# Optimization experiments

Hardware: AMD Instinct MI355X
Metric: run time of the kernel (lower is better)

The kernel has to match this reference:

```python
import jax, jax.numpy as jnp
import numpy as np

B, T, S, E, H = 4, 2048, 2048, 512, 8
D = E // H  # head_dim = 64
BIFURCATION_FACTOR = 1.0


def setup_inputs() -> dict:
    key = jax.random.key(0)
    ks = jax.random.split(key, 12)
    s = 1.0 / np.sqrt(E)
    return {
        "query": jax.random.normal(ks[0], (B, T, E), jnp.float32),
        "key_": jax.random.normal(ks[1], (B, S, E), jnp.float32),
        "value": jax.random.normal(ks[2], (B, S, E), jnp.float32),
        "Wq": jax.random.uniform(ks[3], (E, E), jnp.float32, -s, s),
        "bq": jax.random.uniform(ks[4], (E,), jnp.float32, -s, s),
        "Wk": jax.random.uniform(ks[5], (E, E), jnp.float32, -s, s),
        "bk": jax.random.uniform(ks[6], (E,), jnp.float32, -s, s),
        "Wv": jax.random.uniform(ks[7], (E, E), jnp.float32, -s, s),
        "bv": jax.random.uniform(ks[8], (E,), jnp.float32, -s, s),
        "Wo": jax.random.uniform(ks[9], (E, E), jnp.float32, -s, s),
        "bo": jax.random.uniform(ks[10], (E,), jnp.float32, -s, s),
        "r": jnp.asarray(3.5, jnp.float32),
    }


def _logistic_map(x, r):
    # sigmoid-normalize then one logistic-map iteration with learned r
    xn = jax.nn.sigmoid(x)
    r_scaled = BIFURCATION_FACTOR * jax.nn.sigmoid(r) * 4.0
    return r_scaled * xn * (1.0 - xn)


def reference(query, key_, value, Wq, bq, Wk, bk, Wv, bv, Wo, bo, r):
    q = _logistic_map(query @ Wq.T + bq, r)   # [B,T,E]
    k = _logistic_map(key_ @ Wk.T + bk, r)    # [B,S,E]
    v = value @ Wv.T + bv                     # [B,S,E]

    q = q.reshape(B, T, H, D).transpose(0, 2, 1, 3)  # [B,H,T,D]
    k = k.reshape(B, S, H, D).transpose(0, 2, 1, 3)  # [B,H,S,D]
    v = v.reshape(B, S, H, D).transpose(0, 2, 1, 3)  # [B,H,S,D]

    scores = jnp.einsum('bhtd,bhsd->bhts', q, k) / jnp.sqrt(jnp.asarray(D, q.dtype))
    attn = jax.nn.softmax(scores, axis=-1)           # [B,H,T,S]
    out = jnp.einsum('bhts,bhsd->bhtd', attn, v)     # [B,H,T,D]
    out = out.transpose(0, 2, 1, 3).reshape(B, T, E)
    return out @ Wo.T + bo
```

## Files before the change

### kernel.cpp

```cpp
#include <hip/hip_runtime.h>
#include <stdint.h>

#define B_ 4
#define T_ 2048
#define S_ 2048
#define E_ 512
#define H_ 8
#define D_ 64

using bf16x8 = __attribute__((ext_vector_type(8))) short;
using bf16x4 = __attribute__((ext_vector_type(4))) short;
using f32x4  = __attribute__((ext_vector_type(4))) float;

__device__ __forceinline__ unsigned short f2bf(float f) {
  unsigned u = __float_as_uint(f);
  u += 0x7fffu + ((u >> 16) & 1u);
  return (unsigned short)(u >> 16);
}

__device__ __forceinline__ float sigmoidf_(float x) {
  return 1.0f / (1.0f + __expf(-x));
}

__device__ __forceinline__ f32x4 mfma16x16x16(bf16x4 a, bf16x4 b, f32x4 c) {
#if __has_builtin(__builtin_amdgcn_mfma_f32_16x16x16bf16_1k)
  return __builtin_amdgcn_mfma_f32_16x16x16bf16_1k(a, b, c, 0, 0, 0);
#else
  asm("v_mfma_f32_16x16x16_bf16 %0, %1, %2, %0" : "+v"(c) : "v"(a), "v"(b));
  return c;
#endif
}

__device__ __forceinline__ void gl16(const void* g, void* l) {
  __builtin_amdgcn_global_load_lds(
      (const __attribute__((address_space(1))) unsigned*)g,
      (__attribute__((address_space(3))) unsigned*)l,
      16, 0, 0);
}

__device__ __forceinline__ int swzi(int row, int ebyte) {
  return row * 64 + ((ebyte ^ ((row & 7) << 4)) >> 1);
}

__global__ __launch_bounds__(256) void cvt_all(
    const float* __restrict__ q, const float* __restrict__ k, const float* __restrict__ v,
    const float* __restrict__ wq, const float* __restrict__ wk,
    const float* __restrict__ wv, const float* __restrict__ wo,
    unsigned short* __restrict__ oq, unsigned short* __restrict__ ok,
    unsigned short* __restrict__ ov, unsigned short* __restrict__ owq,
    unsigned short* __restrict__ owk, unsigned short* __restrict__ owv,
    unsigned short* __restrict__ owo) {
  const float* in; unsigned short* out; int n4, b, nb;
  int blk = blockIdx.x;
  if (blk < 1536) {
    int s = blk >> 9;
    in = (s == 0) ? q : (s == 1) ? k : v;
    out = (s == 0) ? oq : (s == 1) ? ok : ov;
    n4 = (B_ * T_ * E_) / 4; b = blk & 511; nb = 512;
  } else {
    int s = (blk - 1536) >> 5;
    in = (s == 0) ? wq : (s == 1) ? wk : (s == 2) ? wv : wo;
    out = (s == 0) ? owq : (s == 1) ? owk : (s == 2) ? owv : owo;
    n4 = (E_ * E_) / 4; b = (blk - 1536) & 31; nb = 32;
  }
  for (int i = b * 256 + threadIdx.x; i < n4; i += nb * 256) {
    float4 vv = ((const float4*)in)[i];
    ushort4 o;
    o.x = f2bf(vv.x); o.y = f2bf(vv.y); o.z = f2bf(vv.z); o.w = f2bf(vv.w);
    ((ushort4*)out)[i] = o;
  }
}

__global__ __launch_bounds__(256) void gemm_out(
    const unsigned short* __restrict__ A,
    const unsigned short* __restrict__ W,
    const float* __restrict__ bias,
    float* __restrict__ outp) {
  __shared__ unsigned short As[2][128 * 64];
  __shared__ unsigned short Bs[2][64 * 64];

  int bid = ((blockIdx.x & 7) << 6) + (blockIdx.x >> 3);
  int tid = threadIdx.x;
  int lane = tid & 63, wid = tid >> 6;
  int bm = bid >> 3, bn = bid & 7;
  int m0 = bm * 128, n0 = bn * 64;

  f32x4 acc[4][2] = {};

  int rowc = tid >> 3;
  int kswz = ((tid & 7) ^ (rowc & 7)) << 4;

  auto stage = [&](int buf, int kt) {
#pragma unroll
    for (int c = 0; c < 4; ++c) {
      const char* ga = (const char*)A + (size_t)(m0 + c * 32 + rowc) * 1024 + kt * 128 + kswz;
      gl16(ga, (char*)&As[buf][0] + c * 4096 + (wid << 10));
    }
#pragma unroll
    for (int c = 0; c < 2; ++c) {
      const char* gw = (const char*)W + (size_t)(n0 + c * 32 + rowc) * 1024 + kt * 128 + kswz;
      gl16(gw, (char*)&Bs[buf][0] + c * 4096 + (wid << 10));
    }
  };

  stage(0, 0);

  int wm = wid >> 1, wn = wid & 1;
  int fr = lane & 15, fg = lane >> 4;

  for (int kt = 0; kt < 8; ++kt) {
    __syncthreads();
    if (kt < 7) stage((kt + 1) & 1, kt + 1);
    int buf = kt & 1;
#pragma unroll
    for (int ks = 0; ks < 2; ++ks) {
      bf16x8 a[4], b[2];
#pragma unroll
      for (int mi = 0; mi < 4; ++mi)
        a[mi] = *(const bf16x8*)&As[buf][swzi(wm * 64 + mi * 16 + fr, ks * 64 + fg * 16)];
#pragma unroll
      for (int ni = 0; ni < 2; ++ni)
        b[ni] = *(const bf16x8*)&Bs[buf][swzi(wn * 32 + ni * 16 + fr, ks * 64 + fg * 16)];
#pragma unroll
      for (int mi = 0; mi < 4; ++mi)
#pragma unroll
        for (int ni = 0; ni < 2; ++ni)
          acc[mi][ni] = __builtin_amdgcn_mfma_f32_16x16x32_bf16(a[mi], b[ni], acc[mi][ni], 0, 0, 0);
    }
  }

#pragma unroll
  for (int mi = 0; mi < 4; ++mi)
#pragma unroll
    for (int ni = 0; ni < 2; ++ni)
#pragma unroll
      for (int i = 0; i < 4; ++i) {
        int gm = m0 + wm * 64 + mi * 16 + fg * 4 + i;
        int gn = n0 + wn * 32 + ni * 16 + fr;
        outp[(size_t)gm * E_ + gn] = acc[mi][ni][i] + bias[gn];
      }
}

__global__ __launch_bounds__(256) void gemm_proj(
    const unsigned short* __restrict__ Aq, const unsigned short* __restrict__ Wqp,
    const float* __restrict__ bqp, unsigned short* __restrict__ oq,
    const unsigned short* __restrict__ Ak, const unsigned short* __restrict__ Wkp,
    const float* __restrict__ bkp, unsigned short* __restrict__ ok,
    const unsigned short* __restrict__ Av, const unsigned short* __restrict__ Wvp,
    const float* __restrict__ bvp, unsigned short* __restrict__ ov,
    const float* __restrict__ rptr, float sclq) {
  __shared__ unsigned short As[2][128 * 64];
  __shared__ unsigned short Bs[2][64 * 64];

  int job = blockIdx.x >> 9;
  int x = blockIdx.x & 511;
  int bid = ((x & 7) << 6) + (x >> 3);
  const unsigned short* A = (job == 0) ? Aq : (job == 1) ? Ak : Av;
  const unsigned short* W = (job == 0) ? Wqp : (job == 1) ? Wkp : Wvp;
  const float* bias = (job == 0) ? bqp : (job == 1) ? bkp : bvp;
  unsigned short* outp = (job == 0) ? oq : (job == 1) ? ok : ov;

  int bm, bn;
  if (job == 2) { bm = bid >> 7; bn = bid & 127; }
  else          { bm = bid >> 3; bn = bid & 7; }
  int m0 = bm * 128, n0 = bn * 64;

  f32x4 acc[4][2] = {};

  int tid = threadIdx.x;
  int lane = tid & 63, wid = tid >> 6;
  int rowc = tid >> 3;
  int kswz = ((tid & 7) ^ (rowc & 7)) << 4;

  auto stage = [&](int buf, int kt) {
#pragma unroll
    for (int c = 0; c < 4; ++c) {
      const char* ga = (const char*)A + (size_t)(m0 + c * 32 + rowc) * 1024 + kt * 128 + kswz;
      gl16(ga, (char*)&As[buf][0] + c * 4096 + (wid << 10));
    }
#pragma unroll
    for (int c = 0; c < 2; ++c) {
      const char* gw = (const char*)W + (size_t)(n0 + c * 32 + rowc) * 1024 + kt * 128 + kswz;
      gl16(gw, (char*)&Bs[buf][0] + c * 4096 + (wid << 10));
    }
  };

  stage(0, 0);

  int wm = wid >> 1, wn = wid & 1;
  int fr = lane & 15, fg = lane >> 4;

  for (int kt = 0; kt < 8; ++kt) {
    __syncthreads();
    if (kt < 7) stage((kt + 1) & 1, kt + 1);
    int buf = kt & 1;
#pragma unroll
    for (int ks = 0; ks < 2; ++ks) {
      bf16x8 a[4], b[2];
#pragma unroll
      for (int mi = 0; mi < 4; ++mi)
        a[mi] = *(const bf16x8*)&As[buf][swzi(wm * 64 + mi * 16 + fr, ks * 64 + fg * 16)];
#pragma unroll
      for (int ni = 0; ni < 2; ++ni)
        b[ni] = *(const bf16x8*)&Bs[buf][swzi(wn * 32 + ni * 16 + fr, ks * 64 + fg * 16)];
#pragma unroll
      for (int mi = 0; mi < 4; ++mi)
#pragma unroll
        for (int ni = 0; ni < 2; ++ni)
          acc[mi][ni] = __builtin_amdgcn_mfma_f32_16x16x32_bf16(a[mi], b[ni], acc[mi][ni], 0, 0, 0);
    }
  }

  float rs = 4.0f * sigmoidf_(rptr[0]) * ((job == 0) ? sclq : 1.0f);

#pragma unroll
  for (int mi = 0; mi < 4; ++mi) {
#pragma unroll
    for (int ni = 0; ni < 2; ++ni) {
#pragma unroll
      for (int i = 0; i < 4; ++i) {
        int gm = m0 + wm * 64 + mi * 16 + fg * 4 + i;
        int gn = n0 + wn * 32 + ni * 16 + fr;
        float v = acc[mi][ni][i];
        if (job < 2) {
          v += bias[gn];
          float xn = sigmoidf_(v);
          float val = rs * xn * (1.0f - xn);
          int b = gm >> 11, t = gm & 2047, h = gn >> 6, d = gn & 63;
          outp[((size_t)(b * H_ + h) * T_ + t) * D_ + d] = f2bf(val);
        } else {
          v += bias[gm];
          int h = gm >> 6, d = gm & 63, b = gn >> 11, s = gn & 2047;
          outp[((size_t)(b * H_ + h) * D_ + d) * S_ + s] = f2bf(v);
        }
      }
    }
  }
}

template <int CBa, int CBb>
__device__ __forceinline__ void tile_pair(
    char* sm, int koff0, int koff1, const int (&voff)[4],
    const bf16x8 (&qa)[2][2], f32x4 (&acco)[2][4], float (&lst)[2]) {
  union PU { unsigned u[2]; bf16x4 v; };

  bf16x8 ka[4][2];
#pragma unroll
  for (int ni = 0; ni < 4; ++ni) {
    ka[ni][0] = *(const bf16x8*)(sm + CBa + ni * 2048 + koff0);
    ka[ni][1] = *(const bf16x8*)(sm + CBa + ni * 2048 + koff1);
  }
  f32x4 sta[4][2] = {};
  __builtin_amdgcn_s_setprio(1);
#pragma unroll
  for (int ni = 0; ni < 4; ++ni)
#pragma unroll
    for (int mi = 0; mi < 2; ++mi) {
      sta[ni][mi] = __builtin_amdgcn_mfma_f32_16x16x32_bf16(ka[ni][0], qa[mi][0], sta[ni][mi], 0, 0, 0);
      sta[ni][mi] = __builtin_amdgcn_mfma_f32_16x16x32_bf16(ka[ni][1], qa[mi][1], sta[ni][mi], 0, 0, 0);
    }
  __builtin_amdgcn_s_setprio(0);

  bf16x8 kb[4][2];
#pragma unroll
  for (int ni = 0; ni < 4; ++ni) {
    kb[ni][0] = *(const bf16x8*)(sm + CBb + ni * 2048 + koff0);
    kb[ni][1] = *(const bf16x8*)(sm + CBb + ni * 2048 + koff1);
  }
  f32x4 stb[4][2] = {};
  __builtin_amdgcn_s_setprio(1);
#pragma unroll
  for (int ni = 0; ni < 4; ++ni)
#pragma unroll
    for (int mi = 0; mi < 2; ++mi) {
      stb[ni][mi] = __builtin_amdgcn_mfma_f32_16x16x32_bf16(kb[ni][0], qa[mi][0], stb[ni][mi], 0, 0, 0);
      stb[ni][mi] = __builtin_amdgcn_mfma_f32_16x16x32_bf16(kb[ni][1], qa[mi][1], stb[ni][mi], 0, 0, 0);
    }
  __builtin_amdgcn_s_setprio(0);

  bf16x4 pfa[2][4];
#pragma unroll
  for (int mi = 0; mi < 2; ++mi) {
    float sum = 0.f;
#pragma unroll
    for (int ni = 0; ni < 4; ++ni) {
      float p0 = __builtin_amdgcn_exp2f(sta[ni][mi][0]);
      float p1 = __builtin_amdgcn_exp2f(sta[ni][mi][1]);
      float p2 = __builtin_amdgcn_exp2f(sta[ni][mi][2]);
      float p3 = __builtin_amdgcn_exp2f(sta[ni][mi][3]);
      sum += (p0 + p1) + (p2 + p3);
      PU pu;
      asm("v_cvt_pk_bf16_f32 %0, %1, %2" : "=v"(pu.u[0]) : "v"(p0), "v"(p1));
      asm("v_cvt_pk_bf16_f32 %0, %1, %2" : "=v"(pu.u[1]) : "v"(p2), "v"(p3));
      pfa[mi][ni] = pu.v;
    }
    sum += __shfl_xor(sum, 16);
    sum += __shfl_xor(sum, 32);
    lst[mi] += sum;
  }

  __builtin_amdgcn_s_setprio(1);
#pragma unroll
  for (int nd = 0; nd < 4; ++nd)
#pragma unroll
    for (int ni = 0; ni < 4; ++ni) {
      bf16x4 vf = *(const bf16x4*)(sm + CBa + nd * 2048 + voff[ni]);
#pragma unroll
      for (int mi = 0; mi < 2; ++mi)
        acco[mi][nd] = mfma16x16x16(vf, pfa[mi][ni], acco[mi][nd]);
    }
  __builtin_amdgcn_s_setprio(0);

  bf16x4 pfb[2][4];
#pragma unroll
  for (int mi = 0; mi < 2; ++mi) {
    float sum = 0.f;
#pragma unroll
    for (int ni = 0; ni < 4; ++ni) {
      float p0 = __builtin_amdgcn_exp2f(stb[ni][mi][0]);
      float p1 = __builtin_amdgcn_exp2f(stb[ni][mi][1]);
      float p2 = __builtin_amdgcn_exp2f(stb[ni][mi][2]);
      float p3 = __builtin_amdgcn_exp2f(stb[ni][mi][3]);
      sum += (p0 + p1) + (p2 + p3);
      PU pu;
      asm("v_cvt_pk_bf16_f32 %0, %1, %2" : "=v"(pu.u[0]) : "v"(p0), "v"(p1));
      asm("v_cvt_pk_bf16_f32 %0, %1, %2" : "=v"(pu.u[1]) : "v"(p2), "v"(p3));
      pfb[mi][ni] = pu.v;
    }
    sum += __shfl_xor(sum, 16);
    sum += __shfl_xor(sum, 32);
    lst[mi] += sum;
  }

  __builtin_amdgcn_s_setprio(1);
#pragma unroll
  for (int nd = 0; nd < 4; ++nd)
#pragma unroll
    for (int ni = 0; ni < 4; ++ni) {
      bf16x4 vf = *(const bf16x4*)(sm + CBb + nd * 2048 + voff[ni]);
#pragma unroll
      for (int mi = 0; mi < 2; ++mi)
        acco[mi][nd] = mfma16x16x16(vf, pfb[mi][ni], acco[mi][nd]);
    }
  __builtin_amdgcn_s_setprio(0);
}

__global__ __launch_bounds__(256) void attn_flash(
    const unsigned short* __restrict__ qp,
    const unsigned short* __restrict__ kp,
    const unsigned short* __restrict__ vtp,
    unsigned short* __restrict__ attno) {
  __shared__ __align__(16) char smem[65536];

  int tid = threadIdx.x, lane = tid & 63, wid = tid >> 6;
  int wgid = ((blockIdx.x & 7) << 6) + (blockIdx.x >> 3);
  int tt = wgid & 15, bh = wgid >> 4;
  const char* qh = (const char*)qp + ((size_t)bh * T_ + tt * 128) * 128;
  const char* kh = (const char*)kp + (size_t)bh * S_ * 128;
  const char* vh = (const char*)vtp + (size_t)bh * D_ * S_ * 2;

  int rowc = tid >> 3;
  int kswz = ((tid & 7) ^ (rowc & 7)) << 4;

#define STAGE_K(SB, IT) { \
    gl16(kh + (size_t)((IT) * 64 + rowc) * 128 + kswz, smem + (SB) + (wid << 10)); \
    gl16(kh + (size_t)((IT) * 64 + 32 + rowc) * 128 + kswz, smem + (SB) + 4096 + (wid << 10)); }
#define STAGE_V(SB, IT) { \
    gl16(vh + (size_t)rowc * 4096 + (IT) * 128 + kswz, smem + (SB) + 8192 + (wid << 10)); \
    gl16(vh + (size_t)(32 + rowc) * 4096 + (IT) * 128 + kswz, smem + (SB) + 12288 + (wid << 10)); }

  STAGE_K(0, 0) STAGE_V(0, 0) STAGE_K(16384, 1) STAGE_V(16384, 1)
#pragma unroll
  for (int c = 0; c < 4; ++c)
    gl16(qh + (size_t)(c * 32 + rowc) * 128 + kswz, smem + 49152 + c * 4096 + (wid << 10));

  int fr = lane & 15, fg = (lane >> 4) & 3;
  int qrb = wid * 32;
  int koff0 = fr * 128 + ((fg * 16) ^ ((fr & 7) << 4));
  int koff1 = fr * 128 + ((64 + fg * 16) ^ ((fr & 7) << 4));
  int voff[4];
#pragma unroll
  for (int ni = 0; ni < 4; ++ni)
    voff[ni] = 8192 + fr * 128 + ((ni * 32 + fg * 8) ^ ((fr & 7) << 4));

  __syncthreads();

  bf16x8 qa[2][2];
#pragma unroll
  for (int mi = 0; mi < 2; ++mi) {
    qa[mi][0] = *(const bf16x8*)(smem + 49152 + (qrb + mi * 16) * 128 + koff0);
    qa[mi][1] = *(const bf16x8*)(smem + 49152 + (qrb + mi * 16) * 128 + koff1);
  }
  __syncthreads();

  f32x4 acco[2][4] = {};
  float lst[2] = {0.f, 0.f};

  STAGE_K(32768, 2) STAGE_V(32768, 2) STAGE_K(49152, 3) STAGE_V(49152, 3)
  tile_pair<0, 16384>(smem, koff0, koff1, voff, qa, acco, lst);

#pragma unroll 1
  for (int pp = 1; pp <= 7; ++pp) {
    int ta = pp * 4;
    __syncthreads();
    STAGE_K(0, ta) STAGE_V(0, ta) STAGE_K(16384, ta + 1) STAGE_V(16384, ta + 1)
    tile_pair<32768, 49152>(smem, koff0, koff1, voff, qa, acco, lst);
    __syncthreads();
    STAGE_K(32768, ta + 2) STAGE_V(32768, ta + 2) STAGE_K(49152, ta + 3) STAGE_V(49152, ta + 3)
    tile_pair<0, 16384>(smem, koff0, koff1, voff, qa, acco, lst);
  }
  __syncthreads();
  tile_pair<32768, 49152>(smem, koff0, koff1, voff, qa, acco, lst);

  int b = bh >> 3, h = bh & 7;
#pragma unroll
  for (int mi = 0; mi < 2; ++mi) {
    float rl = 1.0f / lst[mi];
    int t = tt * 128 + qrb + mi * 16 + fr;
    unsigned short* rowp = attno + (size_t)(b * T_ + t) * E_ + h * 64;
#pragma unroll
    for (int nd = 0; nd < 4; ++nd) {
      ushort4 o;
      o.x = f2bf(acco[mi][nd][0] * rl);
      o.y = f2bf(acco[mi][nd][1] * rl);
      o.z = f2bf(acco[mi][nd][2] * rl);
      o.w = f2bf(acco[mi][nd][3] * rl);
      *(ushort4*)(rowp + nd * 16 + fg * 4) = o;
    }
  }
#undef STAGE_K
#undef STAGE_V
}

extern "C" void kernel_launch(void* const* d_in, const int* in_sizes, int n_in,
                              void* d_out, int out_size, void* d_ws, size_t ws_size,
                              hipStream_t stream) {
  const float* query = (const float*)d_in[0];
  const float* key_  = (const float*)d_in[1];
  const float* value = (const float*)d_in[2];
  const float* Wq    = (const float*)d_in[3];
  const float* bq    = (const float*)d_in[4];
  const float* Wk    = (const float*)d_in[5];
  const float* bk    = (const float*)d_in[6];
  const float* Wv    = (const float*)d_in[7];
  const float* bv    = (const float*)d_in[8];
  const float* Wo    = (const float*)d_in[9];
  const float* bo    = (const float*)d_in[10];
  const float* r     = (const float*)d_in[11];

  char* ws = (char*)d_ws;
  unsigned short* qb    = (unsigned short*)(ws + 0);
  unsigned short* kb    = (unsigned short*)(ws + 8388608);
  unsigned short* vb    = (unsigned short*)(ws + 16777216);
  unsigned short* wqb   = (unsigned short*)(ws + 25165824);
  unsigned short* wkb   = (unsigned short*)(ws + 25690112);
  unsigned short* wvb   = (unsigned short*)(ws + 26214400);
  unsigned short* wob   = (unsigned short*)(ws + 26738688);
  unsigned short* qp    = (unsigned short*)(ws + 27262976);
  unsigned short* kp    = (unsigned short*)(ws + 35651584);
  unsigned short* vtp   = (unsigned short*)(ws + 44040192);
  unsigned short* attno = (unsigned short*)(ws + 52428800);

  cvt_all<<<1664, 256, 0, stream>>>(query, key_, value, Wq, Wk, Wv, Wo,
                                    qb, kb, vb, wqb, wkb, wvb, wob);

  const float SCLQ = 0.125f * 1.44269504089f;

  gemm_proj<<<1536, 256, 0, stream>>>(qb, wqb, bq, qp,
                                      kb, wkb, bk, kp,
                                      wvb, vb, bv, vtp, r, SCLQ);

  attn_flash<<<512, 256, 0, stream>>>(qp, kp, vtp, attno);

  gemm_out<<<512, 256, 0, stream>>>(attno, wob, bo, (float*)d_out);
}
```

Before: 112.9 us.

## Fuse fp32-to-bf16 conversion into projection GEMM loads, drop cvt kernel

Removes the standalone conversion kernel. The projection and output GEMMs now read fp32 inputs and weights straight from global memory into registers, convert them to bf16 with packed cvt instructions, and write them to swizzled LDS. This saves a full read and write pass over Q/K/V plus one kernel launch. In exchange the async global-to-LDS loads become register-staged loads, which raises register pressure, and each GEMM tile reads twice as many bytes as before.

```diff
diff --git a/kernel.cpp b/kernel.cpp
--- a/kernel.cpp
+++ b/kernel.cpp
@@ -20,6 +20,15 @@
 
 __device__ __forceinline__ float sigmoidf_(float x) {
   return 1.0f / (1.0f + __expf(-x));
+}
+
+__device__ __forceinline__ uint4 cvt8(float4 a, float4 b) {
+  uint4 r;
+  asm("v_cvt_pk_bf16_f32 %0, %1, %2" : "=v"(r.x) : "v"(a.x), "v"(a.y));
+  asm("v_cvt_pk_bf16_f32 %0, %1, %2" : "=v"(r.y) : "v"(a.z), "v"(a.w));
+  asm("v_cvt_pk_bf16_f32 %0, %1, %2" : "=v"(r.z) : "v"(b.x), "v"(b.y));
+  asm("v_cvt_pk_bf16_f32 %0, %1, %2" : "=v"(r.w) : "v"(b.z), "v"(b.w));
+  return r;
 }
 
 __device__ __forceinline__ f32x4 mfma16x16x16(bf16x4 a, bf16x4 b, f32x4 c) {
@@ -42,111 +51,12 @@
   return row * 64 + ((ebyte ^ ((row & 7) << 4)) >> 1);
 }
 
-__global__ __launch_bounds__(256) void cvt_all(
-    const float* __restrict__ q, const float* __restrict__ k, const float* __restrict__ v,
-    const float* __restrict__ wq, const float* __restrict__ wk,
-    const float* __restrict__ wv, const float* __restrict__ wo,
-    unsigned short* __restrict__ oq, unsigned short* __restrict__ ok,
-    unsigned short* __restrict__ ov, unsigned short* __restrict__ owq,
-    unsigned short* __restrict__ owk, unsigned short* __restrict__ owv,
-    unsigned short* __restrict__ owo) {
-  const float* in; unsigned short* out; int n4, b, nb;
-  int blk = blockIdx.x;
-  if (blk < 1536) {
-    int s = blk >> 9;
-    in = (s == 0) ? q : (s == 1) ? k : v;
-    out = (s == 0) ? oq : (s == 1) ? ok : ov;
-    n4 = (B_ * T_ * E_) / 4; b = blk & 511; nb = 512;
-  } else {
-    int s = (blk - 1536) >> 5;
-    in = (s == 0) ? wq : (s == 1) ? wk : (s == 2) ? wv : wo;
-    out = (s == 0) ? owq : (s == 1) ? owk : (s == 2) ? owv : owo;
-    n4 = (E_ * E_) / 4; b = (blk - 1536) & 31; nb = 32;
-  }
-  for (int i = b * 256 + threadIdx.x; i < n4; i += nb * 256) {
-    float4 vv = ((const float4*)in)[i];
-    ushort4 o;
-    o.x = f2bf(vv.x); o.y = f2bf(vv.y); o.z = f2bf(vv.z); o.w = f2bf(vv.w);
-    ((ushort4*)out)[i] = o;
-  }
-}
-
-__global__ __launch_bounds__(256) void gemm_out(
-    const unsigned short* __restrict__ A,
-    const unsigned short* __restrict__ W,
-    const float* __restrict__ bias,
-    float* __restrict__ outp) {
-  __shared__ unsigned short As[2][128 * 64];
-  __shared__ unsigned short Bs[2][64 * 64];
-
-  int bid = ((blockIdx.x & 7) << 6) + (blockIdx.x >> 3);
-  int tid = threadIdx.x;
-  int lane = tid & 63, wid = tid >> 6;
-  int bm = bid >> 3, bn = bid & 7;
-  int m0 = bm * 128, n0 = bn * 64;
-
-  f32x4 acc[4][2] = {};
-
-  int rowc = tid >> 3;
-  int kswz = ((tid & 7) ^ (rowc & 7)) << 4;
-
-  auto stage = [&](int buf, int kt) {
-#pragma unroll
-    for (int c = 0; c < 4; ++c) {
-      const char* ga = (const char*)A + (size_t)(m0 + c * 32 + rowc) * 1024 + kt * 128 + kswz;
-      gl16(ga, (char*)&As[buf][0] + c * 4096 + (wid << 10));
-    }
-#pragma unroll
-    for (int c = 0; c < 2; ++c) {
-      const char* gw = (const char*)W + (size_t)(n0 + c * 32 + rowc) * 1024 + kt * 128 + kswz;
-      gl16(gw, (char*)&Bs[buf][0] + c * 4096 + (wid << 10));
-    }
-  };
-
-  stage(0, 0);
-
-  int wm = wid >> 1, wn = wid & 1;
-  int fr = lane & 15, fg = lane >> 4;
-
-  for (int kt = 0; kt < 8; ++kt) {
-    __syncthreads();
-    if (kt < 7) stage((kt + 1) & 1, kt + 1);
-    int buf = kt & 1;
-#pragma unroll
-    for (int ks = 0; ks < 2; ++ks) {
-      bf16x8 a[4], b[2];
-#pragma unroll
-      for (int mi = 0; mi < 4; ++mi)
-        a[mi] = *(const bf16x8*)&As[buf][swzi(wm * 64 + mi * 16 + fr, ks * 64 + fg * 16)];
-#pragma unroll
-      for (int ni = 0; ni < 2; ++ni)
-        b[ni] = *(const bf16x8*)&Bs[buf][swzi(wn * 32 + ni * 16 + fr, ks * 64 + fg * 16)];
-#pragma unroll
-      for (int mi = 0; mi < 4; ++mi)
-#pragma unroll
-        for (int ni = 0; ni < 2; ++ni)
-          acc[mi][ni] = __builtin_amdgcn_mfma_f32_16x16x32_bf16(a[mi], b[ni], acc[mi][ni], 0, 0, 0);
-    }
-  }
-
-#pragma unroll
-  for (int mi = 0; mi < 4; ++mi)
-#pragma unroll
-    for (int ni = 0; ni < 2; ++ni)
-#pragma unroll
-      for (int i = 0; i < 4; ++i) {
-        int gm = m0 + wm * 64 + mi * 16 + fg * 4 + i;
-        int gn = n0 + wn * 32 + ni * 16 + fr;
-        outp[(size_t)gm * E_ + gn] = acc[mi][ni][i] + bias[gn];
-      }
-}
-
 __global__ __launch_bounds__(256) void gemm_proj(
-    const unsigned short* __restrict__ Aq, const unsigned short* __restrict__ Wqp,
+    const float* __restrict__ Aq, const float* __restrict__ Wqf,
     const float* __restrict__ bqp, unsigned short* __restrict__ oq,
-    const unsigned short* __restrict__ Ak, const unsigned short* __restrict__ Wkp,
+    const float* __restrict__ Ak, const float* __restrict__ Wkf,
     const float* __restrict__ bkp, unsigned short* __restrict__ ok,
-    const unsigned short* __restrict__ Av, const unsigned short* __restrict__ Wvp,
+    const float* __restrict__ Wvf, const float* __restrict__ Av,
     const float* __restrict__ bvp, unsigned short* __restrict__ ov,
     const float* __restrict__ rptr, float sclq) {
   __shared__ unsigned short As[2][128 * 64];
@@ -155,8 +65,8 @@
   int job = blockIdx.x >> 9;
   int x = blockIdx.x & 511;
   int bid = ((x & 7) << 6) + (x >> 3);
-  const unsigned short* A = (job == 0) ? Aq : (job == 1) ? Ak : Av;
-  const unsigned short* W = (job == 0) ? Wqp : (job == 1) ? Wkp : Wvp;
+  const float* A = (job == 0) ? Aq : (job == 1) ? Ak : Wvf;
+  const float* W = (job == 0) ? Wqf : (job == 1) ? Wkf : Av;
   const float* bias = (job == 0) ? bqp : (job == 1) ? bkp : bvp;
   unsigned short* outp = (job == 0) ? oq : (job == 1) ? ok : ov;
 
@@ -169,30 +79,45 @@
 
   int tid = threadIdx.x;
   int lane = tid & 63, wid = tid >> 6;
-  int rowc = tid >> 3;
-  int kswz = ((tid & 7) ^ (rowc & 7)) << 4;
-
-  auto stage = [&](int buf, int kt) {
+  int rowc = tid >> 3, slot = tid & 7;
+  int fcol = (slot ^ (rowc & 7)) << 3;
+
+  float4 lva[8], lvb[4];
+  auto LOAD = [&](int kt) {
 #pragma unroll
     for (int c = 0; c < 4; ++c) {
-      const char* ga = (const char*)A + (size_t)(m0 + c * 32 + rowc) * 1024 + kt * 128 + kswz;
-      gl16(ga, (char*)&As[buf][0] + c * 4096 + (wid << 10));
+      const float* g = A + (size_t)(m0 + c * 32 + rowc) * 512 + kt * 64 + fcol;
+      lva[c * 2] = *(const float4*)g;
+      lva[c * 2 + 1] = *(const float4*)(g + 4);
     }
 #pragma unroll
     for (int c = 0; c < 2; ++c) {
-      const char* gw = (const char*)W + (size_t)(n0 + c * 32 + rowc) * 1024 + kt * 128 + kswz;
-      gl16(gw, (char*)&Bs[buf][0] + c * 4096 + (wid << 10));
+      const float* g = W + (size_t)(n0 + c * 32 + rowc) * 512 + kt * 64 + fcol;
+      lvb[c * 2] = *(const float4*)g;
+      lvb[c * 2 + 1] = *(const float4*)(g + 4);
     }
   };
-
-  stage(0, 0);
+  auto WRITE = [&](int buf) {
+#pragma unroll
+    for (int c = 0; c < 4; ++c)
+      *(uint4*)((char*)&As[buf][0] + c * 4096 + rowc * 128 + slot * 16) =
+          cvt8(lva[c * 2], lva[c * 2 + 1]);
+#pragma unroll
+    for (int c = 0; c < 2; ++c)
+      *(uint4*)((char*)&Bs[buf][0] + c * 4096 + rowc * 128 + slot * 16) =
+          cvt8(lvb[c * 2], lvb[c * 2 + 1]);
+  };
+
+  LOAD(0);
+  WRITE(0);
 
   int wm = wid >> 1, wn = wid & 1;
   int fr = lane & 15, fg = lane >> 4;
 
+#pragma unroll 1
   for (int kt = 0; kt < 8; ++kt) {
     __syncthreads();
-    if (kt < 7) stage((kt + 1) & 1, kt + 1);
+    if (kt < 7) LOAD(kt + 1);
     int buf = kt & 1;
 #pragma unroll
     for (int ks = 0; ks < 2; ++ks) {
@@ -209,6 +134,7 @@
         for (int ni = 0; ni < 2; ++ni)
           acc[mi][ni] = __builtin_amdgcn_mfma_f32_16x16x32_bf16(a[mi], b[ni], acc[mi][ni], 0, 0, 0);
     }
+    if (kt < 7) WRITE((kt + 1) & 1);
   }
 
   float rs = 4.0f * sigmoidf_(rptr[0]) * ((job == 0) ? sclq : 1.0f);
@@ -238,6 +164,91 @@
   }
 }
 
+__global__ __launch_bounds__(256) void gemm_out(
+    const unsigned short* __restrict__ A,
+    const float* __restrict__ Wf,
+    const float* __restrict__ bias,
+    float* __restrict__ outp) {
+  __shared__ unsigned short As[2][128 * 64];
+  __shared__ unsigned short Bs[2][64 * 64];
+
+  int bid = ((blockIdx.x & 7) << 6) + (blockIdx.x >> 3);
+  int tid = threadIdx.x;
+  int lane = tid & 63, wid = tid >> 6;
+  int bm = bid >> 3, bn = bid & 7;
+  int m0 = bm * 128, n0 = bn * 64;
+
+  f32x4 acc[4][2] = {};
+
+  int rowc = tid >> 3, slot = tid & 7;
+  int kswz = (slot ^ (rowc & 7)) << 4;
+  int fcol = (slot ^ (rowc & 7)) << 3;
+
+  auto stageA = [&](int buf, int kt) {
+#pragma unroll
+    for (int c = 0; c < 4; ++c) {
+      const char* ga = (const char*)A + (size_t)(m0 + c * 32 + rowc) * 1024 + kt * 128 + kswz;
+      gl16(ga, (char*)&As[buf][0] + c * 4096 + (wid << 10));
+    }
+  };
+  float4 lvb[4];
+  auto LOADW = [&](int kt) {
+#pragma unroll
+    for (int c = 0; c < 2; ++c) {
+      const float* g = Wf + (size_t)(n0 + c * 32 + rowc) * 512 + kt * 64 + fcol;
+      lvb[c * 2] = *(const float4*)g;
+      lvb[c * 2 + 1] = *(const float4*)(g + 4);
+    }
+  };
+  auto WRITEW = [&](int buf) {
+#pragma unroll
+    for (int c = 0; c < 2; ++c)
+      *(uint4*)((char*)&Bs[buf][0] + c * 4096 + rowc * 128 + slot * 16) =
+          cvt8(lvb[c * 2], lvb[c * 2 + 1]);
+  };
+
+  stageA(0, 0);
+  LOADW(0);
+  WRITEW(0);
+
+  int wm = wid >> 1, wn = wid & 1;
+  int fr = lane & 15, fg = lane >> 4;
+
+#pragma unroll 1
+  for (int kt = 0; kt < 8; ++kt) {
+    __syncthreads();
+    if (kt < 7) { stageA((kt + 1) & 1, kt + 1); LOADW(kt + 1); }
+    int buf = kt & 1;
+#pragma unroll
+    for (int ks = 0; ks < 2; ++ks) {
+      bf16x8 a[4], b[2];
+#pragma unroll
+      for (int mi = 0; mi < 4; ++mi)
+        a[mi] = *(const bf16x8*)&As[buf][swzi(wm * 64 + mi * 16 + fr, ks * 64 + fg * 16)];
+#pragma unroll
+      for (int ni = 0; ni < 2; ++ni)
+        b[ni] = *(const bf16x8*)&Bs[buf][swzi(wn * 32 + ni * 16 + fr, ks * 64 + fg * 16)];
+#pragma unroll
+      for (int mi = 0; mi < 4; ++mi)
+#pragma unroll
+        for (int ni = 0; ni < 2; ++ni)
+          acc[mi][ni] = __builtin_amdgcn_mfma_f32_16x16x32_bf16(a[mi], b[ni], acc[mi][ni], 0, 0, 0);
+    }
+    if (kt < 7) WRITEW((kt + 1) & 1);
+  }
+
+#pragma unroll
+  for (int mi = 0; mi < 4; ++mi)
+#pragma unroll
+    for (int ni = 0; ni < 2; ++ni)
+#pragma unroll
+      for (int i = 0; i < 4; ++i) {
+        int gm = m0 + wm * 64 + mi * 16 + fg * 4 + i;
+        int gn = n0 + wn * 32 + ni * 16 + fr;
+        outp[(size_t)gm * E_ + gn] = acc[mi][ni][i] + bias[gn];
+      }
+}
+
 template <int CBa, int CBb>
 __device__ __forceinline__ void tile_pair(
     char* sm, int koff0, int koff1, const int (&voff)[4],
@@ -449,28 +460,18 @@
   const float* r     = (const float*)d_in[11];
 
   char* ws = (char*)d_ws;
-  unsigned short* qb    = (unsigned short*)(ws + 0);
-  unsigned short* kb    = (unsigned short*)(ws + 8388608);
-  unsigned short* vb    = (unsigned short*)(ws + 16777216);
-  unsigned short* wqb   = (unsigned short*)(ws + 25165824);
-  unsigned short* wkb   = (unsigned short*)(ws + 25690112);
-  unsigned short* wvb   = (unsigned short*)(ws + 26214400);
-  unsigned short* wob   = (unsigned short*)(ws + 26738688);
   unsigned short* qp    = (unsigned short*)(ws + 27262976);
   unsigned short* kp    = (unsigned short*)(ws + 35651584);
   unsigned short* vtp   = (unsigned short*)(ws + 44040192);
   unsigned short* attno = (unsigned short*)(ws + 52428800);
 
-  cvt_all<<<1664, 256, 0, stream>>>(query, key_, value, Wq, Wk, Wv, Wo,
-                                    qb, kb, vb, wqb, wkb, wvb, wob);
-
   const float SCLQ = 0.125f * 1.44269504089f;
 
-  gemm_proj<<<1536, 256, 0, stream>>>(qb, wqb, bq, qp,
-                                      kb, wkb, bk, kp,
-                                      wvb, vb, bv, vtp, r, SCLQ);
+  gemm_proj<<<1536, 256, 0, stream>>>(query, Wq, bq, qp,
+                                      key_, Wk, bk, kp,
+                                      Wv, value, bv, vtp, r, SCLQ);
 
   attn_flash<<<512, 256, 0, stream>>>(qp, kp, vtp, attno);
 
-  gemm_out<<<512, 256, 0, stream>>>(attno, wob, bo, (float*)d_out);
-}
+  gemm_out<<<512, 256, 0, stream>>>(attno, Wo, bo, (float*)d_out);
+}
```

Measured after the change: 112.5 us (median of 2 runs). About the same (-0.3%).
